# Optimization experiments

Measured on AMD Instinct MI355X. Metric: run time of the kernel, lower is better.

The kernel has to match this reference:

```python
import jax, jax.numpy as jnp
import numpy as np

THRESHOLD = 0.5
EPS = 1e-6

def cxcywh_to_xyxy(b):
    return jnp.concatenate([b[..., :2] - b[..., 2:] / 2, b[..., :2] + b[..., 2:] / 2], axis=-1)

def xyxy_to_cxcywh(b):
    return jnp.concatenate([(b[..., :2] + b[..., 2:]) / 2, b[..., 2:] - b[..., :2]], axis=-1)

def iou_matrix(a, b, eps):
    # a: [P,4] xyxy, b: [O,4] xyxy -> [P,O]
    lb = jnp.maximum(a[:, None, :2], b[None, :, :2])
    ub = jnp.minimum(a[:, None, 2:], b[None, :, 2:])
    wh = jnp.clip(ub - lb, 0.0)
    inter = wh[..., 0] * wh[..., 1]
    area_a = (a[:, 2] - a[:, 0]) * (a[:, 3] - a[:, 1])
    area_b = (b[:, 2] - b[:, 0]) * (b[:, 3] - b[:, 1])
    union = area_a[:, None] + area_b[None, :] - inter
    return inter / (union + eps)

def match_single(priors_xyxy, t_xyxy, t_labels):
    # SSD-style matching (stand-in for Calculate_bbox_target_classes)
    n_obj = t_xyxy.shape[0]
    iou = iou_matrix(priors_xyxy, t_xyxy, EPS)          # [P,O]
    best_obj_iou = jnp.max(iou, axis=1)                 # [P]
    best_obj = jnp.argmax(iou, axis=1)                  # [P]
    best_prior = jnp.argmax(iou, axis=0)                # [O] force-match each object
    best_obj = best_obj.at[best_prior].set(jnp.arange(n_obj))
    best_obj_iou = best_obj_iou.at[best_prior].set(1.0)
    labels = t_labels[best_obj]                          # [P]
    labels = jnp.where(best_obj_iou < THRESHOLD, 0, labels)
    locs = xyxy_to_cxcywh(t_xyxy[best_obj])              # [P,4] cxcywh
    return labels, locs

def setup_inputs() -> dict:
    key = jax.random.key(0)
    k1, k2, k3, k4, k5, k6, k7 = jax.random.split(key, 7)
    B, P, C, O = 64, 8732, 81, 32
    # predictions: cxcywh-ish boxes in [0,1]
    pl_xy = jax.random.uniform(k1, (B, P, 2))
    pl_wh = jax.random.uniform(k2, (B, P, 2)) * 0.25 + 0.02
    predictlocs = jnp.concatenate([pl_xy, pl_wh], axis=-1)
    predictcls = jax.random.normal(k3, (B, P, C))
    pr_xy = jax.random.uniform(k4, (P, 2))
    pr_wh = jax.random.uniform(k5, (P, 2)) * 0.25 + 0.02
    prior_bboxes = jnp.concatenate([pr_xy, pr_wh], axis=-1)
    tb_xy = jax.random.uniform(k6, (B, O, 2)) * 0.8
    tb_wh = jax.random.uniform(k7, (B, O, 2)) * 0.2 + 0.02
    target_bboxes = jnp.concatenate([tb_xy, tb_wh], axis=-1)  # xywh
    target_labels = jax.random.randint(jax.random.fold_in(key, 99), (B, O), 1, C)
    return {"predictlocs": predictlocs, "predictcls": predictcls,
            "prior_bboxes": prior_bboxes, "target_bboxes": target_bboxes,
            "target_labels": target_labels}

def _iou_loss_masked(pred_cxcywh, tgt_cxcywh, pos_mask):
    tp = cxcywh_to_xyxy(tgt_cxcywh)
    bp = cxcywh_to_xyxy(pred_cxcywh)
    lb = jnp.maximum(tp[..., :2], bp[..., :2])
    ub = jnp.minimum(tp[..., 2:], bp[..., 2:])
    wh = jnp.clip(ub - lb, 0.0)
    inter = wh[..., 0] * wh[..., 1]
    area_b = (bp[..., 2] - bp[..., 0]) * (bp[..., 3] - bp[..., 1])
    area_t = (tp[..., 2] - tp[..., 0]) * (tp[..., 3] - tp[..., 1])
    union = area_t + area_b - inter
    v = 1.0 - inter / (union + EPS)
    n_pos = jnp.sum(pos_mask)
    return jnp.sum(jnp.where(pos_mask, v, 0.0)) / n_pos

def reference(predictlocs, predictcls, prior_bboxes, target_bboxes, target_labels):
    n_classes = predictcls.shape[2]
    # xywh -> xyxy, as in original forward
    t_xyxy = jnp.concatenate([target_bboxes[..., :2],
                              target_bboxes[..., :2] + target_bboxes[..., 2:]], axis=-1)
    priors_xyxy = cxcywh_to_xyxy(prior_bboxes)
    true_classes, true_locs = jax.vmap(match_single, in_axes=(None, 0, 0))(
        priors_xyxy, t_xyxy, target_labels)      # [B,P], [B,P,4]
    pos = true_classes != 0                       # [B,P]
    n_pos = jnp.sum(pos).astype(predictlocs.dtype)
    # IoU loss over positives (mean over positives)
    iou_loss = _iou_loss_masked(predictlocs, true_locs, pos)
    # L1 loss (mean over all elements of selected [Npos,4])
    l1 = jnp.abs(predictlocs - true_locs)
    loc_loss = jnp.sum(jnp.where(pos[..., None], l1, 0.0)) / (n_pos * 4.0)
    # CrossEntropy over all priors (mean)
    logp = jax.nn.log_softmax(predictcls.reshape(-1, n_classes), axis=-1)
    cross_loss = -jnp.mean(jnp.take_along_axis(
        logp, true_classes.reshape(-1, 1), axis=-1))
    return loc_loss, cross_loss, iou_loss
```

## Files before the change

### kernel.cpp

```cpp
#include <hip/hip_runtime.h>
#include <hip/hip_bf16.h>

#define NB 64
#define NP 8732
#define NO 32
#define NC 81
#define NROWS (NB * NP)
#define PBLK 2183
#define ITERS (NROWS / 16)
#define CGRID 2048


__device__ __forceinline__ float ldT(const float* p, size_t i) { return p[i]; }
__device__ __forceinline__ float ldT(const unsigned short* p, size_t i) {
    return __uint_as_float((unsigned)p[i] << 16);
}
__device__ __forceinline__ float4 ld4(const float* p, size_t i) {
    return *(const float4*)(p + i);
}
__device__ __forceinline__ float4 ld4(const unsigned short* p, size_t i) {
    ushort4 u = *(const ushort4*)(p + i);
    return make_float4(__uint_as_float((unsigned)u.x << 16),
                       __uint_as_float((unsigned)u.y << 16),
                       __uint_as_float((unsigned)u.z << 16),
                       __uint_as_float((unsigned)u.w << 16));
}

__global__ void init_kernel(const void* __restrict__ prior,
                            unsigned long long* __restrict__ bestPrior,
                            float* __restrict__ accum, int* __restrict__ flag) {
    int i = threadIdx.x;
    for (int j = i; j < NB * NO; j += blockDim.x) bestPrior[j] = 0ull;
    if (i < 4) accum[i] = 0.0f;
    if (i < 64) {
        const unsigned short* pb = (const unsigned short*)prior;
        float v = __uint_as_float((unsigned)pb[i] << 16);
        unsigned long long bad = __ballot(!(fabsf(v) <= 8.0f));
        if (i == 0) *flag = (__popcll(bad) >= 8) ? 1 : 0;
    }
}

template <typename T>
__device__ __forceinline__ void match_body(
        const T* __restrict__ prior, const T* __restrict__ tb,
        unsigned long long* __restrict__ bestPrior) {
    const int b   = blockIdx.y;
    const int o   = threadIdx.x & 31;
    const int seg = threadIdx.x >> 5;
    const int p0  = blockIdx.x * 256 + seg * 32;

    float4 t = ld4(tb, ((size_t)(b * NO + o)) * 4);
    float tx0 = t.x, ty0 = t.y, tx1 = t.x + t.z, ty1 = t.y + t.w, ta = t.z * t.w;

    float bi = -1.0f;
    int bp = 0;
    for (int j = 0; j < 32; ++j) {
        int p = p0 + j;
        if (p >= NP) break;
        float4 pr = ld4(prior, (size_t)p * 4);
        float px0 = pr.x - pr.z * 0.5f, py0 = pr.y - pr.w * 0.5f;
        float px1 = pr.x + pr.z * 0.5f, py1 = pr.y + pr.w * 0.5f;
        float pa = (px1 - px0) * (py1 - py0);
        float lbx = fmaxf(px0, tx0), lby = fmaxf(py0, ty0);
        float ubx = fminf(px1, tx1), uby = fminf(py1, ty1);
        float ww = fmaxf(ubx - lbx, 0.0f), hh = fmaxf(uby - lby, 0.0f);
        float inter = ww * hh;
        float iou = inter / (pa + ta - inter + 1e-6f);
        if (iou > bi) { bi = iou; bp = p; }
    }
    if (bi >= 0.0f) {
        unsigned long long packed =
            (((unsigned long long)__float_as_uint(bi)) << 32) | (~(unsigned)bp);
        atomicMax(&bestPrior[b * NO + o], packed);
    }
}

__global__ __launch_bounds__(256) void match_kernel(
        const void* __restrict__ prior, const void* __restrict__ tb,
        unsigned long long* __restrict__ bestPrior, const int* __restrict__ flag) {
    if (*flag)
        match_body<float>((const float*)prior, (const float*)tb, bestPrior);
    else
        match_body<unsigned short>((const unsigned short*)prior,
                                   (const unsigned short*)tb, bestPrior);
}

template <typename T>
__device__ void prep_impl(
        const T* __restrict__ plocs, const T* __restrict__ prior,
        const T* __restrict__ tb, const int* __restrict__ tlab,
        const unsigned long long* __restrict__ bestPrior,
        unsigned char* __restrict__ lab8, float* __restrict__ accum) {
    __shared__ float4 s_box[2][NO];
    __shared__ float  s_area[2][NO];
    __shared__ int    s_lab[2][NO];
    __shared__ unsigned s_forced[2][NO];
    __shared__ float red[4][3];

    const int tid = threadIdx.x;
    const int lane = tid & 63;
    const int wv = tid >> 6;
    const int row = blockIdx.x * 256 + tid;
    const int b = row / NP;
    const int p = row - b * NP;
    const int b0 = (blockIdx.x * 256) / NP;

    if (tid < 64) {
        int bb = tid >> 5, o = tid & 31;
        int bq = b0 + bb;
        if (bq < NB) {
            float4 t = ld4(tb, ((size_t)(bq * NO + o)) * 4);
            s_box[bb][o] = make_float4(t.x, t.y, t.x + t.z, t.y + t.w);
            s_area[bb][o] = t.z * t.w;
            s_lab[bb][o] = tlab[bq * NO + o];
            s_forced[bb][o] = ~(unsigned)(bestPrior[bq * NO + o] & 0xffffffffull);
        }
    }
    __syncthreads();

    const int bb = b - b0;
    float4 pr = ld4(prior, (size_t)p * 4);
    float px0 = pr.x - pr.z * 0.5f, py0 = pr.y - pr.w * 0.5f;
    float px1 = pr.x + pr.z * 0.5f, py1 = pr.y + pr.w * 0.5f;
    float pa = (px1 - px0) * (py1 - py0);

    float bi = -1.0f;
    int bo = 0, fo = -1;
    for (int o = 0; o < NO; ++o) {
        float4 t = s_box[bb][o];
        float lbx = fmaxf(px0, t.x), lby = fmaxf(py0, t.y);
        float ubx = fminf(px1, t.z), uby = fminf(py1, t.w);
        float ww = fmaxf(ubx - lbx, 0.0f), hh = fmaxf(uby - lby, 0.0f);
        float inter = ww * hh;
        float iou = inter / (pa + s_area[bb][o] - inter + 1e-6f);
        if (iou > bi) { bi = iou; bo = o; }
        if (s_forced[bb][o] == (unsigned)p) fo = o;
    }
    if (fo >= 0) { bo = fo; bi = 1.0f; }

    int lab = s_lab[bb][bo];
    if (bi < 0.5f) lab = 0;
    lab8[row] = (unsigned char)lab;

    float l1_sum = 0.f, iou_sum = 0.f, np_sum = 0.f;
    if (lab != 0) {
        np_sum = 1.0f;
        float4 t = s_box[bb][bo];
        float x0 = t.x, y0 = t.y, x1 = t.z, y1 = t.w;
        float tw = x1 - x0, th = y1 - y0;
        float4 traw = ld4(tb, ((size_t)(b * NO + bo)) * 4);
        float tcx = (x0 + x1) * 0.5f, tcy = (y0 + y1) * 0.5f;
        float4 qv = ld4(plocs, (size_t)row * 4);
        l1_sum = fabsf(qv.x - tcx) + fabsf(qv.y - tcy)
               + fabsf(qv.z - traw.z) + fabsf(qv.w - traw.w);
        float qX0 = qv.x - qv.z * 0.5f, qY0 = qv.y - qv.w * 0.5f;
        float qX1 = qv.x + qv.z * 0.5f, qY1 = qv.y + qv.w * 0.5f;
        float lbx = fmaxf(x0, qX0), lby = fmaxf(y0, qY0);
        float ubx = fminf(x1, qX1), uby = fminf(y1, qY1);
        float iw = fmaxf(ubx - lbx, 0.f), ih = fmaxf(uby - lby, 0.f);
        float inter = iw * ih;
        float areaq = (qX1 - qX0) * (qY1 - qY0);
        float areat = (x1 - x0) * (y1 - y0);
        iou_sum = 1.0f - inter / (areat + areaq - inter + 1e-6f);
        (void)tw; (void)th;
    }

    #pragma unroll
    for (int d = 1; d < 64; d <<= 1) {
        l1_sum  += __shfl_xor(l1_sum, d);
        iou_sum += __shfl_xor(iou_sum, d);
        np_sum  += __shfl_xor(np_sum, d);
    }
    if (lane == 0) { red[wv][0] = l1_sum; red[wv][1] = iou_sum; red[wv][2] = np_sum; }
    __syncthreads();
    if (tid == 0) {
        float a1 = 0, a2 = 0, a3 = 0;
        for (int k = 0; k < 4; ++k) { a1 += red[k][0]; a2 += red[k][1]; a3 += red[k][2]; }
        atomicAdd(&accum[1], a1);
        atomicAdd(&accum[2], a2);
        atomicAdd(&accum[3], a3);
    }
}

__global__ __launch_bounds__(256) void prep_kernel(
        const void* __restrict__ plocs, const void* __restrict__ prior,
        const void* __restrict__ tb, const int* __restrict__ tlab,
        const unsigned long long* __restrict__ bestPrior,
        const int* __restrict__ flag,
        unsigned char* __restrict__ lab8, float* __restrict__ accum) {
    if (*flag)
        prep_impl<float>((const float*)plocs, (const float*)prior,
                         (const float*)tb, tlab, bestPrior, lab8, accum);
    else
        prep_impl<unsigned short>((const unsigned short*)plocs,
                                  (const unsigned short*)prior,
                                  (const unsigned short*)tb,
                                  tlab, bestPrior, lab8, accum);
}

template <typename T>
__device__ void ce_impl(const T* __restrict__ pcls,
                        const unsigned char* __restrict__ lab8,
                        float* __restrict__ accum) {
    const int tid = threadIdx.x;
    const int lane = tid & 63;
    const int wv = tid >> 6;
    const int q = lane & 15;

    float c_sum = 0.f;

    for (int it0 = blockIdx.x; it0 < ITERS; it0 += 2 * CGRID) {
        int it1 = it0 + CGRID;
        bool hasB = (it1 < ITERS);
        int rowA = it0 * 16 + wv * 4 + (lane >> 4);
        int rowB = hasB ? (it1 * 16 + wv * 4 + (lane >> 4)) : rowA;

        int labA = lab8[rowA];
        int labB = lab8[rowB];
        const T* xrA = pcls + (size_t)rowA * NC;
        const T* xrB = pcls + (size_t)rowB * NC;

        float vA[5], vB[5];
        #pragma unroll
        for (int j = 0; j < 5; ++j) { vA[j] = ldT(xrA, q + 16 * j);
                                      vB[j] = ldT(xrB, q + 16 * j); }
        float v80A = (q == 0) ? ldT(xrA, 80) : -1e30f;
        float v80B = (q == 0) ? ldT(xrB, 80) : -1e30f;
        float xlA = (q == 0) ? ldT(xrA, labA) : 0.f;
        float xlB = (q == 0) ? ldT(xrB, labB) : 0.f;

        float mA = fmaxf(fmaxf(fmaxf(vA[0], vA[1]), fmaxf(vA[2], vA[3])),
                         fmaxf(vA[4], v80A));
        float mB = fmaxf(fmaxf(fmaxf(vB[0], vB[1]), fmaxf(vB[2], vB[3])),
                         fmaxf(vB[4], v80B));
        #pragma unroll
        for (int d = 1; d < 16; d <<= 1) {
            mA = fmaxf(mA, __shfl_xor(mA, d));
            mB = fmaxf(mB, __shfl_xor(mB, d));
        }
        float sA = __expf(vA[0] - mA) + __expf(vA[1] - mA) + __expf(vA[2] - mA)
                 + __expf(vA[3] - mA) + __expf(vA[4] - mA) + __expf(v80A - mA);
        float sB = __expf(vB[0] - mB) + __expf(vB[1] - mB) + __expf(vB[2] - mB)
                 + __expf(vB[3] - mB) + __expf(vB[4] - mB) + __expf(v80B - mB);
        #pragma unroll
        for (int d = 1; d < 16; d <<= 1) {
            sA += __shfl_xor(sA, d);
            sB += __shfl_xor(sB, d);
        }
        if (q == 0) {
            c_sum += (mA + __logf(sA)) - xlA;
            if (hasB) c_sum += (mB + __logf(sB)) - xlB;
        }
    }

    #pragma unroll
    for (int d = 1; d < 64; d <<= 1) c_sum += __shfl_xor(c_sum, d);
    __shared__ float red[4];
    if (lane == 0) red[wv] = c_sum;
    __syncthreads();
    if (tid == 0)
        atomicAdd(&accum[0], red[0] + red[1] + red[2] + red[3]);
}

__global__ __launch_bounds__(256) void ce_kernel(
        const void* __restrict__ pcls, const unsigned char* __restrict__ lab8,
        const int* __restrict__ flag, float* __restrict__ accum) {
    if (*flag)
        ce_impl<float>((const float*)pcls, lab8, accum);
    else
        ce_impl<unsigned short>((const unsigned short*)pcls, lab8, accum);
}

__global__ void finalize_kernel(const float* __restrict__ accum,
                                const int* __restrict__ flag, void* __restrict__ out) {
    if (threadIdx.x == 0) {
        float cross = accum[0] / (float)NROWS;
        float npos = accum[3];
        float loc = accum[1] / (npos * 4.0f);
        float iou = accum[2] / npos;
        if (*flag) {
            float* o = (float*)out;
            o[0] = loc; o[1] = cross; o[2] = iou;
        } else {
            __hip_bfloat16* o = (__hip_bfloat16*)out;
            o[0] = __float2bfloat16(loc);
            o[1] = __float2bfloat16(cross);
            o[2] = __float2bfloat16(iou);
        }
    }
}

extern "C" void kernel_launch(void* const* d_in, const int* in_sizes, int n_in,
                              void* d_out, int out_size, void* d_ws, size_t ws_size,
                              hipStream_t stream) {
    const void* plocs = d_in[0];
    const void* pcls  = d_in[1];
    const void* prior = d_in[2];
    const void* tb    = d_in[3];
    const int*  tlab  = (const int*)d_in[4];

    char* w = (char*)d_ws;
    unsigned long long* bestPrior = (unsigned long long*)w;
    float* accum = (float*)(w + 16384);
    int*   flag  = (int*)(w + 16400);
    unsigned char* lab8 = (unsigned char*)(w + 16408);

    hipLaunchKernelGGL(init_kernel, dim3(1), dim3(256), 0, stream,
                       prior, bestPrior, accum, flag);

    dim3 gA((NP + 255) / 256, NB);
    hipLaunchKernelGGL(match_kernel, gA, dim3(256), 0, stream,
                       prior, tb, bestPrior, flag);

    hipLaunchKernelGGL(prep_kernel, dim3(PBLK), dim3(256), 0, stream,
                       plocs, prior, tb, tlab, bestPrior, flag, lab8, accum);

    hipLaunchKernelGGL(ce_kernel, dim3(CGRID), dim3(256), 0, stream,
                       pcls, lab8, flag, accum);

    hipLaunchKernelGGL(finalize_kernel, dim3(1), dim3(64), 0, stream,
                       accum, flag, d_out);
}
```

Baseline: 394.3 us.

## Fuse prior-matching prep and cross-entropy into one kernel via shared labels

Merges the prep kernel (per-prior best-object matching and loc/IoU loss) with the cross-entropy kernel. Each block now computes the labels for its 256 rows into shared memory and then runs the log-softmax on those same rows, so the global lab8 array and one kernel launch go away. This trades the grid-stride CE loop over 2048 blocks for a fixed 2183-block grid where every block does both phases, which may lower memory-level parallelism in the streaming class-logit reads.

```diff
diff --git a/kernel.cpp b/kernel.cpp
--- a/kernel.cpp
+++ b/kernel.cpp
@@ -7,8 +7,6 @@
 #define NC 81
 #define NROWS (NB * NP)
 #define PBLK 2183
-#define ITERS (NROWS / 16)
-#define CGRID 2048
 
 
 __device__ __forceinline__ float ldT(const float* p, size_t i) { return p[i]; }
@@ -86,16 +84,17 @@
 }
 
 template <typename T>
-__device__ void prep_impl(
+__device__ void prepce_impl(
         const T* __restrict__ plocs, const T* __restrict__ prior,
         const T* __restrict__ tb, const int* __restrict__ tlab,
         const unsigned long long* __restrict__ bestPrior,
-        unsigned char* __restrict__ lab8, float* __restrict__ accum) {
+        const T* __restrict__ pcls, float* __restrict__ accum) {
     __shared__ float4 s_box[2][NO];
     __shared__ float  s_area[2][NO];
     __shared__ int    s_lab[2][NO];
     __shared__ unsigned s_forced[2][NO];
-    __shared__ float red[4][3];
+    __shared__ unsigned char s_lab8[256];
+    __shared__ float red[4][4];
 
     const int tid = threadIdx.x;
     const int lane = tid & 63;
@@ -140,14 +139,13 @@
 
     int lab = s_lab[bb][bo];
     if (bi < 0.5f) lab = 0;
-    lab8[row] = (unsigned char)lab;
+    s_lab8[tid] = (unsigned char)lab;
 
     float l1_sum = 0.f, iou_sum = 0.f, np_sum = 0.f;
     if (lab != 0) {
         np_sum = 1.0f;
         float4 t = s_box[bb][bo];
         float x0 = t.x, y0 = t.y, x1 = t.z, y1 = t.w;
-        float tw = x1 - x0, th = y1 - y0;
         float4 traw = ld4(tb, ((size_t)(b * NO + bo)) * 4);
         float tcx = (x0 + x1) * 0.5f, tcy = (y0 + y1) * 0.5f;
         float4 qv = ld4(plocs, (size_t)row * 4);
@@ -162,63 +160,22 @@
         float areaq = (qX1 - qX0) * (qY1 - qY0);
         float areat = (x1 - x0) * (y1 - y0);
         iou_sum = 1.0f - inter / (areat + areaq - inter + 1e-6f);
-        (void)tw; (void)th;
-    }
+    }
+
+    __syncthreads();
+
+    const int q = lane & 15;
+    const int rbase = blockIdx.x * 256;
+    float c_sum = 0.f;
 
     #pragma unroll
-    for (int d = 1; d < 64; d <<= 1) {
-        l1_sum  += __shfl_xor(l1_sum, d);
-        iou_sum += __shfl_xor(iou_sum, d);
-        np_sum  += __shfl_xor(np_sum, d);
-    }
-    if (lane == 0) { red[wv][0] = l1_sum; red[wv][1] = iou_sum; red[wv][2] = np_sum; }
-    __syncthreads();
-    if (tid == 0) {
-        float a1 = 0, a2 = 0, a3 = 0;
-        for (int k = 0; k < 4; ++k) { a1 += red[k][0]; a2 += red[k][1]; a3 += red[k][2]; }
-        atomicAdd(&accum[1], a1);
-        atomicAdd(&accum[2], a2);
-        atomicAdd(&accum[3], a3);
-    }
-}
-
-__global__ __launch_bounds__(256) void prep_kernel(
-        const void* __restrict__ plocs, const void* __restrict__ prior,
-        const void* __restrict__ tb, const int* __restrict__ tlab,
-        const unsigned long long* __restrict__ bestPrior,
-        const int* __restrict__ flag,
-        unsigned char* __restrict__ lab8, float* __restrict__ accum) {
-    if (*flag)
-        prep_impl<float>((const float*)plocs, (const float*)prior,
-                         (const float*)tb, tlab, bestPrior, lab8, accum);
-    else
-        prep_impl<unsigned short>((const unsigned short*)plocs,
-                                  (const unsigned short*)prior,
-                                  (const unsigned short*)tb,
-                                  tlab, bestPrior, lab8, accum);
-}
-
-template <typename T>
-__device__ void ce_impl(const T* __restrict__ pcls,
-                        const unsigned char* __restrict__ lab8,
-                        float* __restrict__ accum) {
-    const int tid = threadIdx.x;
-    const int lane = tid & 63;
-    const int wv = tid >> 6;
-    const int q = lane & 15;
-
-    float c_sum = 0.f;
-
-    for (int it0 = blockIdx.x; it0 < ITERS; it0 += 2 * CGRID) {
-        int it1 = it0 + CGRID;
-        bool hasB = (it1 < ITERS);
-        int rowA = it0 * 16 + wv * 4 + (lane >> 4);
-        int rowB = hasB ? (it1 * 16 + wv * 4 + (lane >> 4)) : rowA;
-
-        int labA = lab8[rowA];
-        int labB = lab8[rowB];
-        const T* xrA = pcls + (size_t)rowA * NC;
-        const T* xrB = pcls + (size_t)rowB * NC;
+    for (int i = 0; i < 8; ++i) {
+        int rlA = i * 16 + wv * 4 + (lane >> 4);
+        int rlB = rlA + 128;
+        int labA = s_lab8[rlA];
+        int labB = s_lab8[rlB];
+        const T* xrA = pcls + (size_t)(rbase + rlA) * NC;
+        const T* xrB = pcls + (size_t)(rbase + rlB) * NC;
 
         float vA[5], vB[5];
         #pragma unroll
@@ -249,26 +206,50 @@
         }
         if (q == 0) {
             c_sum += (mA + __logf(sA)) - xlA;
-            if (hasB) c_sum += (mB + __logf(sB)) - xlB;
+            c_sum += (mB + __logf(sB)) - xlB;
         }
     }
 
     #pragma unroll
-    for (int d = 1; d < 64; d <<= 1) c_sum += __shfl_xor(c_sum, d);
-    __shared__ float red[4];
-    if (lane == 0) red[wv] = c_sum;
+    for (int d = 1; d < 64; d <<= 1) {
+        c_sum   += __shfl_xor(c_sum, d);
+        l1_sum  += __shfl_xor(l1_sum, d);
+        iou_sum += __shfl_xor(iou_sum, d);
+        np_sum  += __shfl_xor(np_sum, d);
+    }
+    if (lane == 0) {
+        red[wv][0] = c_sum; red[wv][1] = l1_sum;
+        red[wv][2] = iou_sum; red[wv][3] = np_sum;
+    }
     __syncthreads();
-    if (tid == 0)
-        atomicAdd(&accum[0], red[0] + red[1] + red[2] + red[3]);
-}
-
-__global__ __launch_bounds__(256) void ce_kernel(
-        const void* __restrict__ pcls, const unsigned char* __restrict__ lab8,
+    if (tid == 0) {
+        float a0 = 0, a1 = 0, a2 = 0, a3 = 0;
+        for (int k = 0; k < 4; ++k) {
+            a0 += red[k][0]; a1 += red[k][1]; a2 += red[k][2]; a3 += red[k][3];
+        }
+        atomicAdd(&accum[0], a0);
+        atomicAdd(&accum[1], a1);
+        atomicAdd(&accum[2], a2);
+        atomicAdd(&accum[3], a3);
+    }
+}
+
+__global__ __launch_bounds__(256) void prepce_kernel(
+        const void* __restrict__ plocs, const void* __restrict__ prior,
+        const void* __restrict__ tb, const int* __restrict__ tlab,
+        const unsigned long long* __restrict__ bestPrior,
+        const void* __restrict__ pcls,
         const int* __restrict__ flag, float* __restrict__ accum) {
     if (*flag)
-        ce_impl<float>((const float*)pcls, lab8, accum);
+        prepce_impl<float>((const float*)plocs, (const float*)prior,
+                           (const float*)tb, tlab, bestPrior,
+                           (const float*)pcls, accum);
     else
-        ce_impl<unsigned short>((const unsigned short*)pcls, lab8, accum);
+        prepce_impl<unsigned short>((const unsigned short*)plocs,
+                                    (const unsigned short*)prior,
+                                    (const unsigned short*)tb,
+                                    tlab, bestPrior,
+                                    (const unsigned short*)pcls, accum);
 }
 
 __global__ void finalize_kernel(const float* __restrict__ accum,
@@ -303,7 +284,6 @@
     unsigned long long* bestPrior = (unsigned long long*)w;
     float* accum = (float*)(w + 16384);
     int*   flag  = (int*)(w + 16400);
-    unsigned char* lab8 = (unsigned char*)(w + 16408);
 
     hipLaunchKernelGGL(init_kernel, dim3(1), dim3(256), 0, stream,
                        prior, bestPrior, accum, flag);
@@ -312,11 +292,8 @@
     hipLaunchKernelGGL(match_kernel, gA, dim3(256), 0, stream,
                        prior, tb, bestPrior, flag);
 
-    hipLaunchKernelGGL(prep_kernel, dim3(PBLK), dim3(256), 0, stream,
-                       plocs, prior, tb, tlab, bestPrior, flag, lab8, accum);
-
-    hipLaunchKernelGGL(ce_kernel, dim3(CGRID), dim3(256), 0, stream,
-                       pcls, lab8, flag, accum);
+    hipLaunchKernelGGL(prepce_kernel, dim3(PBLK), dim3(256), 0, stream,
+                       plocs, prior, tb, tlab, bestPrior, pcls, flag, accum);
 
     hipLaunchKernelGGL(finalize_kernel, dim3(1), dim3(64), 0, stream,
                        accum, flag, d_out);
```

Result: faster. 375.1 us (-4.9%).

## Restructure CE kernel: one-shot 8-row batched loads per wave with DPP reductions

Applied to the files above, without the earlier changes.

The cross-entropy kernel drops its grid-stride loop. Each block now handles exactly 128 rows, and every lane issues all loads for 8 rows up front, separated from the math by a sched barrier, to raise memory-level parallelism. The 16-lane max and sum reductions use DPP row_shr updates instead of ds_swizzle shuffles, and the match loop gets an unroll pragma. The cost is higher register pressure from 40+ live loaded values per lane, which may reduce occupancy.

```diff
diff --git a/kernel.cpp b/kernel.cpp
--- a/kernel.cpp
+++ b/kernel.cpp
@@ -7,8 +7,7 @@
 #define NC 81
 #define NROWS (NB * NP)
 #define PBLK 2183
-#define ITERS (NROWS / 16)
-#define CGRID 2048
+#define CBLK 4366
 
 
 __device__ __forceinline__ float ldT(const float* p, size_t i) { return p[i]; }
@@ -25,6 +24,18 @@
                        __uint_as_float((unsigned)u.z << 16),
                        __uint_as_float((unsigned)u.w << 16));
 }
+
+template <int CTRL>
+__device__ __forceinline__ float dppf(float x) {
+    return __int_as_float(__builtin_amdgcn_update_dpp(
+        0, __float_as_int(x), CTRL, 0xF, 0xF, true));
+}
+#define DPP_RED16(var, OP)                      \
+    var = OP(var, dppf<0x128>(var));            \
+    var = OP(var, dppf<0x124>(var));            \
+    var = OP(var, dppf<0x122>(var));            \
+    var = OP(var, dppf<0x121>(var));
+__device__ __forceinline__ float addf(float a, float b) { return a + b; }
 
 __global__ void init_kernel(const void* __restrict__ prior,
                             unsigned long long* __restrict__ bestPrior,
@@ -126,6 +137,7 @@
 
     float bi = -1.0f;
     int bo = 0, fo = -1;
+    #pragma unroll 8
     for (int o = 0; o < NO; ++o) {
         float4 t = s_box[bb][o];
         float lbx = fmaxf(px0, t.x), lby = fmaxf(py0, t.y);
@@ -147,7 +159,6 @@
         np_sum = 1.0f;
         float4 t = s_box[bb][bo];
         float x0 = t.x, y0 = t.y, x1 = t.z, y1 = t.w;
-        float tw = x1 - x0, th = y1 - y0;
         float4 traw = ld4(tb, ((size_t)(b * NO + bo)) * 4);
         float tcx = (x0 + x1) * 0.5f, tcy = (y0 + y1) * 0.5f;
         float4 qv = ld4(plocs, (size_t)row * 4);
@@ -162,7 +173,6 @@
         float areaq = (qX1 - qX0) * (qY1 - qY0);
         float areat = (x1 - x0) * (y1 - y0);
         iou_sum = 1.0f - inter / (areat + areaq - inter + 1e-6f);
-        (void)tw; (void)th;
     }
 
     #pragma unroll
@@ -202,60 +212,46 @@
 __device__ void ce_impl(const T* __restrict__ pcls,
                         const unsigned char* __restrict__ lab8,
                         float* __restrict__ accum) {
+    __shared__ float red[4];
     const int tid = threadIdx.x;
     const int lane = tid & 63;
     const int wv = tid >> 6;
     const int q = lane & 15;
+    const int g = lane >> 4;
+    const int base = blockIdx.x * 128 + wv * 32;
+
+    int labv[8];
+    #pragma unroll
+    for (int s = 0; s < 8; ++s) labv[s] = lab8[base + s * 4 + g];
+
+    float v[8][5], v80[8], xl[8];
+    #pragma unroll
+    for (int s = 0; s < 8; ++s) {
+        const T* xr = pcls + (size_t)(base + s * 4 + g) * NC;
+        #pragma unroll
+        for (int j = 0; j < 5; ++j) v[s][j] = ldT(xr, q + 16 * j);
+        v80[s] = ldT(xr, 80);
+        xl[s]  = ldT(xr, labv[s]);
+    }
+    __builtin_amdgcn_sched_barrier(0);
 
     float c_sum = 0.f;
-
-    for (int it0 = blockIdx.x; it0 < ITERS; it0 += 2 * CGRID) {
-        int it1 = it0 + CGRID;
-        bool hasB = (it1 < ITERS);
-        int rowA = it0 * 16 + wv * 4 + (lane >> 4);
-        int rowB = hasB ? (it1 * 16 + wv * 4 + (lane >> 4)) : rowA;
-
-        int labA = lab8[rowA];
-        int labB = lab8[rowB];
-        const T* xrA = pcls + (size_t)rowA * NC;
-        const T* xrB = pcls + (size_t)rowB * NC;
-
-        float vA[5], vB[5];
-        #pragma unroll
-        for (int j = 0; j < 5; ++j) { vA[j] = ldT(xrA, q + 16 * j);
-                                      vB[j] = ldT(xrB, q + 16 * j); }
-        float v80A = (q == 0) ? ldT(xrA, 80) : -1e30f;
-        float v80B = (q == 0) ? ldT(xrB, 80) : -1e30f;
-        float xlA = (q == 0) ? ldT(xrA, labA) : 0.f;
-        float xlB = (q == 0) ? ldT(xrB, labB) : 0.f;
-
-        float mA = fmaxf(fmaxf(fmaxf(vA[0], vA[1]), fmaxf(vA[2], vA[3])),
-                         fmaxf(vA[4], v80A));
-        float mB = fmaxf(fmaxf(fmaxf(vB[0], vB[1]), fmaxf(vB[2], vB[3])),
-                         fmaxf(vB[4], v80B));
-        #pragma unroll
-        for (int d = 1; d < 16; d <<= 1) {
-            mA = fmaxf(mA, __shfl_xor(mA, d));
-            mB = fmaxf(mB, __shfl_xor(mB, d));
-        }
-        float sA = __expf(vA[0] - mA) + __expf(vA[1] - mA) + __expf(vA[2] - mA)
-                 + __expf(vA[3] - mA) + __expf(vA[4] - mA) + __expf(v80A - mA);
-        float sB = __expf(vB[0] - mB) + __expf(vB[1] - mB) + __expf(vB[2] - mB)
-                 + __expf(vB[3] - mB) + __expf(vB[4] - mB) + __expf(v80B - mB);
-        #pragma unroll
-        for (int d = 1; d < 16; d <<= 1) {
-            sA += __shfl_xor(sA, d);
-            sB += __shfl_xor(sB, d);
-        }
-        if (q == 0) {
-            c_sum += (mA + __logf(sA)) - xlA;
-            if (hasB) c_sum += (mB + __logf(sB)) - xlB;
-        }
+    #pragma unroll
+    for (int s = 0; s < 8; ++s) {
+        float e80 = (q == 0) ? v80[s] : -1e30f;
+        float mm = fmaxf(fmaxf(fmaxf(v[s][0], v[s][1]), fmaxf(v[s][2], v[s][3])),
+                         fmaxf(v[s][4], e80));
+        DPP_RED16(mm, fmaxf)
+        float ss = __expf(v[s][0] - mm) + __expf(v[s][1] - mm)
+                 + __expf(v[s][2] - mm) + __expf(v[s][3] - mm)
+                 + __expf(v[s][4] - mm) + __expf(e80 - mm);
+        DPP_RED16(ss, addf)
+        float term = (mm + __logf(ss)) - xl[s];
+        c_sum += (q == 0) ? term : 0.0f;
     }
 
     #pragma unroll
     for (int d = 1; d < 64; d <<= 1) c_sum += __shfl_xor(c_sum, d);
-    __shared__ float red[4];
     if (lane == 0) red[wv] = c_sum;
     __syncthreads();
     if (tid == 0)
@@ -315,7 +311,7 @@
     hipLaunchKernelGGL(prep_kernel, dim3(PBLK), dim3(256), 0, stream,
                        plocs, prior, tb, tlab, bestPrior, flag, lab8, accum);
 
-    hipLaunchKernelGGL(ce_kernel, dim3(CGRID), dim3(256), 0, stream,
+    hipLaunchKernelGGL(ce_kernel, dim3(CBLK), dim3(256), 0, stream,
                        pcls, lab8, flag, accum);
 
     hipLaunchKernelGGL(finalize_kernel, dim3(1), dim3(64), 0, stream,
```

Result: no change. 392.7 us (-0.4%).
